# Performance work log

Hardware: AMD Instinct MI355X
Metric: run time of the kernel (lower is better)

Reference implementation:

```python
import jax, jax.numpy as jnp
import numpy as np

K = 3      # kernel size (hardcoded 3x3 in the torch module via repeat(...,9,...))
PAD = 1
STRIDE = 1


def _unfold(x):
    # torch.nn.functional.unfold equivalent: (B,C,H,W) -> (B,C,K,K,oh,ow)
    B, C, H, W = x.shape
    p = jax.lax.conv_general_dilated_patches(
        x, (K, K), (STRIDE, STRIDE), ((PAD, PAD), (PAD, PAD)))
    oh, ow = p.shape[2], p.shape[3]
    return p.reshape(B, C, K, K, oh, ow)


def setup_inputs() -> dict:
    key = jax.random.key(0)
    k1, k2, k3, k4 = jax.random.split(key, 4)
    B, Cin, Cout, H, W = 4, 64, 64, 128, 128
    inputs = jax.random.normal(k1, (B, Cin, H, W), jnp.float32)
    depth = jax.random.uniform(k2, (B, 1, H, W), jnp.float32)  # positive depths
    weight = jax.random.uniform(k3, (K, Cout, Cin, K, K), jnp.float32, minval=-0.05, maxval=0.05)
    bias = jax.random.uniform(k4, (Cout,), jnp.float32, minval=-0.05, maxval=0.05)
    return {"inputs": inputs, "depth": depth, "weight": weight, "bias": bias, "f": 1}


def reference(inputs, depth, weight, bias, f):
    # --- DepthKernelFn: per-depth-plane binary masks ---
    depth_wins = _unfold(depth)          # (B,1,K,K,oh,ow)
    s_wins = depth_wins / f              # grid spacing s_i = d / f
    cy, cx = K // 2, K // 2
    d0 = depth_wins[:, :, cy, cx]        # center depth      (B,1,oh,ow)
    s0 = s_wins[:, :, cy, cx]            # center spacing    (B,1,oh,ow)
    offs = jnp.arange(K, dtype=inputs.dtype) - (K - 1) / 2.0  # l - (K-1)/2
    # z_l at center: d0 + (l-1)*s0  -> (K,B,1,oh,ow)
    z0 = d0[None] + offs[:, None, None, None, None] * s0[None]
    half = s0[None] / 2
    a = (z0 - half)[:, :, :, None, None]  # (K,B,1,1,1,oh,ow)
    b = (z0 + half)[:, :, :, None, None]
    dw = depth_wins[None]                 # (1,B,1,K,K,oh,ow)
    # mask_l = 1 where a <= depth < b else 0  (same as the where-cascade in torch)
    mask = ((dw >= a) & (dw < b)).astype(inputs.dtype)  # (K,B,1,K,K,oh,ow)

    # --- RepeatKernelConvFn: masked windowed conv via einsum ---
    inp_wins = _unfold(inputs)            # (B,C,K,K,oh,ow)
    x = inp_wins[None] * mask             # (K,B,C,K,K,oh,ow), depth C=1 broadcasts
    out = jnp.einsum('hijklmn,hojkl->iomn', x, weight)
    out = out + bias.reshape(1, -1, 1, 1)
    return out
```

## Files before the change

### kernel.cpp

```cpp
#include <hip/hip_runtime.h>
#include <math.h>

#define B_N  4
#define CIN  64
#define COUT 64
#define H_N  128
#define W_N  128

typedef _Float16 half8 __attribute__((ext_vector_type(8)));
typedef float    f32x4 __attribute__((ext_vector_type(4)));

#define KTOT   1728
#define NSTEP  54
#define WA_BYTES ((size_t)NSTEP * 4 * 64 * 8 * 2)

__global__ void wprep(const float* __restrict__ w, _Float16* __restrict__ wa) {
    int idx = blockIdx.x * 256 + threadIdx.x;
    if (idx >= NSTEP * 4 * 64) return;
    int lane = idx & 63;
    int mt   = (idx >> 6) & 3;
    int s    = idx >> 8;
    int m    = mt * 16 + (lane & 15);
    int kl0  = (lane >> 4) * 8;
    _Float16 v[8];
#pragma unroll
    for (int j = 0; j < 8; ++j) {
        int k = s * 32 + kl0 + j;
        int g = k >> 6;
        int c = k & 63;
        int t = g / 3;
        int h = g % 3;
        v[j] = (_Float16)w[(((size_t)(h * COUT) + m) * CIN + c) * 9 + t];
    }
    *(int4*)&wa[(size_t)idx * 8] = *(int4*)v;
}

#define XS_LINE 64
#define XS_ROW  (66 * XS_LINE)

__global__ __launch_bounds__(256, 4)
void conv_mfma(const float* __restrict__ inp, const float* __restrict__ depth,
               const _Float16* __restrict__ wa, const float* __restrict__ bias,
               const int* __restrict__ fptr, float* __restrict__ out) {
    __shared__ _Float16 Xs[3 * XS_ROW];
    __shared__ unsigned hLds[64];

    int bid  = blockIdx.x;
    int xh   = bid & 1;
    int y    = (bid >> 1) & (H_N - 1);
    int b    = bid >> 8;
    int x0   = xh * 64;
    int tid  = threadIdx.x;
    int lane = tid & 63;
    int mq   = tid >> 6;
    int ln15 = lane & 15;
    int quad = lane >> 4;

    {
        int xl  = tid & 63;
        int cq  = tid >> 6;
        int xi  = xl + 1;
        int key = xi & 7;
#pragma unroll
        for (int dyi = 0; dyi < 3; ++dyi) {
            int yy = y + dyi - 1;
            _Float16 hb[16];
            if (yy >= 0 && yy < H_N) {
                const float* src = inp + (((size_t)b * CIN + cq * 16) * H_N + yy) * W_N + (x0 + xl);
                float tf[16];
#pragma unroll
                for (int cc = 0; cc < 16; ++cc) tf[cc] = src[(size_t)cc * H_N * W_N];
#pragma unroll
                for (int cc = 0; cc < 16; ++cc) hb[cc] = (_Float16)tf[cc];
            } else {
#pragma unroll
                for (int cc = 0; cc < 16; ++cc) hb[cc] = (_Float16)0.f;
            }
            _Float16* dst = &Xs[dyi * XS_ROW + xi * XS_LINE];
            *(int4*)&dst[((cq * 2    ) ^ key) * 8] = *(int4*)&hb[0];
            *(int4*)&dst[((cq * 2 + 1) ^ key) * 8] = *(int4*)&hb[8];
        }
        if (tid < 48) {
            int dyi  = tid >> 4;
            int rem  = tid & 15;
            int side = rem >> 3;
            int ck   = rem & 7;
            int xi2  = side ? 65 : 0;
            int xg   = x0 + xi2 - 1;
            int key2 = xi2 & 7;
            int yy   = y + dyi - 1;
            _Float16 hb[8];
            if (xg >= 0 && xg < W_N && yy >= 0 && yy < H_N) {
                const float* src = inp + (((size_t)b * CIN + ck * 8) * H_N + yy) * W_N + xg;
#pragma unroll
                for (int cc = 0; cc < 8; ++cc) hb[cc] = (_Float16)src[(size_t)cc * H_N * W_N];
            } else {
#pragma unroll
                for (int cc = 0; cc < 8; ++cc) hb[cc] = (_Float16)0.f;
            }
            *(int4*)&Xs[dyi * XS_ROW + xi2 * XS_LINE + (ck ^ key2) * 8] = *(int4*)&hb[0];
        }
    }

    const half8* wa8 = (const half8*)wa;
    half8 Abuf[2][6];
    {
        const half8* bA = wa8 + (size_t)mq * 64 + lane;
#pragma unroll
        for (int j = 0; j < 6; ++j) Abuf[0][j] = bA[(size_t)j * 4 * 64];
    }

    if (tid < 64) {
        int x = x0 + tid;
        double fd  = (double)(*fptr);
        float  d0f = depth[((size_t)b * H_N + y) * W_N + x];
        double dd  = (double)d0f;
        double inv = fd / dd;
        bool   pos = (inv > 0.0);
        unsigned pk = 0;
        for (int t = 0; t < 9; ++t) {
            int dy = t / 3 - 1, dx = t % 3 - 1;
            int yy = y + dy, xx = x + dx;
            float dwf = (yy >= 0 && yy < H_N && xx >= 0 && xx < W_N)
                        ? depth[((size_t)b * H_N + yy) * W_N + xx] : 0.f;
            int h = -1;
            if (pos) {
                double u  = ((double)dwf - dd) * inv + 1.5;
                double uf = floor(u);
                if (uf >= 0.0 && uf <= 2.0) h = (int)uf;
            }
            pk |= (unsigned)(h + 1) << (2 * t);
        }
        hLds[tid] = pk;
    }

    __syncthreads();

    unsigned hpk[4];
#pragma unroll
    for (int nt = 0; nt < 4; ++nt) hpk[nt] = hLds[nt * 16 + ln15];

    f32x4 acc[4];
#pragma unroll
    for (int nt = 0; nt < 4; ++nt) acc[nt] = (f32x4){0.f, 0.f, 0.f, 0.f};

    half8 z8 = {(_Float16)0.f, (_Float16)0.f, (_Float16)0.f, (_Float16)0.f,
                (_Float16)0.f, (_Float16)0.f, (_Float16)0.f, (_Float16)0.f};

#pragma unroll
    for (int t = 0; t < 9; ++t) {
        int dyi = t / 3;
        int dx  = t % 3 - 1;

        half8 bb[8];
#pragma unroll
        for (int nt = 0; nt < 4; ++nt) {
            int xs = nt * 16 + ln15 + dx + 1;
            int k2 = xs & 7;
            int ba = dyi * XS_ROW + xs * XS_LINE;
            bb[nt * 2 + 0] = *(const half8*)&Xs[ba + ((quad    ) ^ k2) * 8];
            bb[nt * 2 + 1] = *(const half8*)&Xs[ba + ((quad + 4) ^ k2) * 8];
        }

        if (t < 8) {
            const half8* bA = wa8 + ((size_t)(t + 1) * 24 + mq) * 64 + lane;
#pragma unroll
            for (int j = 0; j < 6; ++j) Abuf[(t + 1) & 1][j] = bA[(size_t)j * 4 * 64];
        }

        int hb[4];
#pragma unroll
        for (int nt = 0; nt < 4; ++nt) hb[nt] = (hpk[nt] >> (2 * t)) & 3;

#pragma unroll
        for (int h = 0; h < 3; ++h) {
#pragma unroll
            for (int kk = 0; kk < 2; ++kk) {
                int j = h * 2 + kk;
#pragma unroll
                for (int nt = 0; nt < 4; ++nt) {
                    half8 c = (hb[nt] == h + 1) ? bb[nt * 2 + kk] : z8;
                    acc[nt] = __builtin_amdgcn_mfma_f32_16x16x32_f16(Abuf[t & 1][j], c, acc[nt], 0, 0, 0);
                }
            }
        }
    }

#pragma unroll
    for (int nt = 0; nt < 4; ++nt) {
        int x = x0 + nt * 16 + ln15;
#pragma unroll
        for (int r = 0; r < 4; ++r) {
            int o = mq * 16 + quad * 4 + r;
            out[(((size_t)b * COUT + o) * H_N + y) * W_N + x] = acc[nt][r] + bias[o];
        }
    }
}

__global__ __launch_bounds__(256)
void conv25d(const float* __restrict__ inp, const float* __restrict__ depth,
             const float* __restrict__ wsrc, const float* __restrict__ bias,
             const int* __restrict__ fptr, float* __restrict__ out) {
    int bid = blockIdx.x;
    int xt  = bid & 3;
    int y   = (bid >> 2) & (H_N - 1);
    int b   = bid >> 9;
    int o   = threadIdx.x & 63;
    int q   = threadIdx.x >> 6;
    int x0  = xt * 32 + q * 8;
    double fd = (double)(*fptr);
    float acc[8];
    float bv = bias[o];
#pragma unroll
    for (int i = 0; i < 8; ++i) acc[i] = bv;
    const float* dcen = depth + ((size_t)b * H_N + y) * W_N;
    float d0[8];
#pragma unroll
    for (int i = 0; i < 8; ++i) d0[i] = dcen[x0 + i];
    for (int t = 0; t < 9; ++t) {
        int dy = t / 3 - 1, dx = t % 3 - 1;
        int yy = y + dy;
        if (yy < 0 || yy >= H_N) continue;
        const float* drow = depth + ((size_t)b * H_N + yy) * W_N;
        int hsel[8];
#pragma unroll
        for (int i = 0; i < 8; ++i) {
            int xx = x0 + i + dx;
            int h = -1;
            if (xx >= 0 && xx < W_N) {
                double dd = (double)d0[i];
                double s0 = dd / fd;
                if (s0 > 0.0) {
                    double u = ((double)drow[xx] - dd) / s0 + 1.5;
                    double uf = floor(u);
                    if (uf >= 0.0 && uf <= 2.0) h = (int)uf;
                }
            }
            hsel[i] = h;
        }
        const float* irow = inp + ((size_t)b * CIN * H_N + yy) * W_N;
        for (int c = 0; c < CIN; ++c) {
            const float* wb = wsrc + ((size_t)o * CIN + c) * 9 + t;
            float w0 = wb[0], w1 = wb[(size_t)COUT * CIN * 9], w2 = wb[2 * (size_t)COUT * CIN * 9];
            const float* ir = irow + (size_t)c * H_N * W_N;
#pragma unroll
            for (int i = 0; i < 8; ++i) {
                int h = hsel[i];
                if (h >= 0) {
                    float wv = (h == 0) ? w0 : ((h == 1) ? w1 : w2);
                    acc[i] = fmaf(ir[x0 + i + dx], wv, acc[i]);
                }
            }
        }
    }
    float* orow = out + (((size_t)b * COUT + o) * H_N + y) * W_N;
#pragma unroll
    for (int i = 0; i < 8; ++i) orow[x0 + i] = acc[i];
}

extern "C" void kernel_launch(void* const* d_in, const int* in_sizes, int n_in,
                              void* d_out, int out_size, void* d_ws, size_t ws_size,
                              hipStream_t stream) {
    const float* inp   = (const float*)d_in[0];
    const float* depth = (const float*)d_in[1];
    const float* w     = (const float*)d_in[2];
    const float* bias  = (const float*)d_in[3];
    const int*   f     = (const int*)d_in[4];
    float* out = (float*)d_out;

    if (ws_size >= WA_BYTES) {
        _Float16* wa = (_Float16*)d_ws;
        wprep<<<NSTEP, 256, 0, stream>>>(w, wa);
        conv_mfma<<<B_N * H_N * 2, 256, 0, stream>>>(inp, depth, wa, bias, f, out);
    } else {
        conv25d<<<B_N * H_N * (W_N / 32), 256, 0, stream>>>(inp, depth, w, bias, f, out);
    }
}
```

Measured before the change: 100.2 us.

## Pipeline input row loads with MFMA compute across kernel rows

```diff
diff --git a/kernel.cpp b/kernel.cpp
--- a/kernel.cpp
+++ b/kernel.cpp
@@ -38,7 +38,7 @@
 #define XS_LINE 64
 #define XS_ROW  (66 * XS_LINE)
 
-__global__ __launch_bounds__(256, 4)
+__global__ __launch_bounds__(256, 3)
 void conv_mfma(const float* __restrict__ inp, const float* __restrict__ depth,
                const _Float16* __restrict__ wa, const float* __restrict__ bias,
                const int* __restrict__ fptr, float* __restrict__ out) {
@@ -56,54 +56,62 @@
     int ln15 = lane & 15;
     int quad = lane >> 4;
 
-    {
-        int xl  = tid & 63;
-        int cq  = tid >> 6;
-        int xi  = xl + 1;
-        int key = xi & 7;
-#pragma unroll
-        for (int dyi = 0; dyi < 3; ++dyi) {
-            int yy = y + dyi - 1;
-            _Float16 hb[16];
-            if (yy >= 0 && yy < H_N) {
-                const float* src = inp + (((size_t)b * CIN + cq * 16) * H_N + yy) * W_N + (x0 + xl);
-                float tf[16];
-#pragma unroll
-                for (int cc = 0; cc < 16; ++cc) tf[cc] = src[(size_t)cc * H_N * W_N];
-#pragma unroll
-                for (int cc = 0; cc < 16; ++cc) hb[cc] = (_Float16)tf[cc];
-            } else {
-#pragma unroll
-                for (int cc = 0; cc < 16; ++cc) hb[cc] = (_Float16)0.f;
-            }
-            _Float16* dst = &Xs[dyi * XS_ROW + xi * XS_LINE];
-            *(int4*)&dst[((cq * 2    ) ^ key) * 8] = *(int4*)&hb[0];
-            *(int4*)&dst[((cq * 2 + 1) ^ key) * 8] = *(int4*)&hb[8];
-        }
-        if (tid < 48) {
-            int dyi  = tid >> 4;
-            int rem  = tid & 15;
-            int side = rem >> 3;
-            int ck   = rem & 7;
-            int xi2  = side ? 65 : 0;
-            int xg   = x0 + xi2 - 1;
-            int key2 = xi2 & 7;
-            int yy   = y + dyi - 1;
-            _Float16 hb[8];
-            if (xg >= 0 && xg < W_N && yy >= 0 && yy < H_N) {
-                const float* src = inp + (((size_t)b * CIN + ck * 8) * H_N + yy) * W_N + xg;
-#pragma unroll
-                for (int cc = 0; cc < 8; ++cc) hb[cc] = (_Float16)src[(size_t)cc * H_N * W_N];
-            } else {
-#pragma unroll
-                for (int cc = 0; cc < 8; ++cc) hb[cc] = (_Float16)0.f;
-            }
-            *(int4*)&Xs[dyi * XS_ROW + xi2 * XS_LINE + (ck ^ key2) * 8] = *(int4*)&hb[0];
-        }
+    int xl   = tid & 63;
+    int cq   = tid >> 6;
+    int xi   = xl + 1;
+    int key  = xi & 7;
+    int side = (tid >> 3) & 1;
+    int ck   = tid & 7;
+    int xi2  = side ? 65 : 0;
+    int xg   = x0 + xi2 - 1;
+    int key2 = xi2 & 7;
+
+    const size_t HW = (size_t)H_N * W_N;
+
+#define LOAD_ROW(dyi, buf, hbuf) {                                            \
+        int yy_ = y + (dyi) - 1;                                              \
+        if (yy_ >= 0 && yy_ < H_N) {                                          \
+            const float* src_ = inp + (((size_t)b * CIN + cq * 16) * H_N + yy_) * W_N + (x0 + xl); \
+            _Pragma("unroll")                                                 \
+            for (int cc = 0; cc < 16; ++cc) buf[cc] = src_[(size_t)cc * HW];  \
+        } else {                                                              \
+            _Pragma("unroll")                                                 \
+            for (int cc = 0; cc < 16; ++cc) buf[cc] = 0.f;                    \
+        }                                                                     \
+        if (tid < 16) {                                                       \
+            if (xg >= 0 && xg < W_N && yy_ >= 0 && yy_ < H_N) {               \
+                const float* hsrc_ = inp + (((size_t)b * CIN + ck * 8) * H_N + yy_) * W_N + xg; \
+                _Pragma("unroll")                                             \
+                for (int cc = 0; cc < 8; ++cc) hbuf[cc] = hsrc_[(size_t)cc * HW]; \
+            } else {                                                          \
+                _Pragma("unroll")                                             \
+                for (int cc = 0; cc < 8; ++cc) hbuf[cc] = 0.f;                \
+            }                                                                 \
+        }                                                                     \
+    }
+
+#define WRITE_ROW(dyi, buf, hbuf) {                                           \
+        _Float16 hb_[16];                                                     \
+        _Pragma("unroll")                                                     \
+        for (int cc = 0; cc < 16; ++cc) hb_[cc] = (_Float16)buf[cc];          \
+        _Float16* dst_ = &Xs[(dyi) * XS_ROW + xi * XS_LINE];                  \
+        *(int4*)&dst_[((cq * 2    ) ^ key) * 8] = *(int4*)&hb_[0];            \
+        *(int4*)&dst_[((cq * 2 + 1) ^ key) * 8] = *(int4*)&hb_[8];            \
+        if (tid < 16) {                                                       \
+            _Float16 hh_[8];                                                  \
+            _Pragma("unroll")                                                 \
+            for (int cc = 0; cc < 8; ++cc) hh_[cc] = (_Float16)hbuf[cc];      \
+            *(int4*)&Xs[(dyi) * XS_ROW + xi2 * XS_LINE + (ck ^ key2) * 8] = *(int4*)&hh_[0]; \
+        }                                                                     \
     }
 
     const half8* wa8 = (const half8*)wa;
     half8 Abuf[2][6];
+
+    float rbuf[16];
+    float rhbuf[8];
+    LOAD_ROW(0, rbuf, rhbuf);
+
     {
         const half8* bA = wa8 + (size_t)mq * 64 + lane;
 #pragma unroll
@@ -134,6 +142,7 @@
         hLds[tid] = pk;
     }
 
+    WRITE_ROW(0, rbuf, rhbuf);
     __syncthreads();
 
     unsigned hpk[4];
@@ -148,51 +157,65 @@
                 (_Float16)0.f, (_Float16)0.f, (_Float16)0.f, (_Float16)0.f};
 
 #pragma unroll
-    for (int t = 0; t < 9; ++t) {
-        int dyi = t / 3;
-        int dx  = t % 3 - 1;
-
-        half8 bb[8];
-#pragma unroll
-        for (int nt = 0; nt < 4; ++nt) {
-            int xs = nt * 16 + ln15 + dx + 1;
-            int k2 = xs & 7;
-            int ba = dyi * XS_ROW + xs * XS_LINE;
-            bb[nt * 2 + 0] = *(const half8*)&Xs[ba + ((quad    ) ^ k2) * 8];
-            bb[nt * 2 + 1] = *(const half8*)&Xs[ba + ((quad + 4) ^ k2) * 8];
-        }
-
-        if (t < 8) {
-            const half8* bA = wa8 + ((size_t)(t + 1) * 24 + mq) * 64 + lane;
-#pragma unroll
-            for (int j = 0; j < 6; ++j) Abuf[(t + 1) & 1][j] = bA[(size_t)j * 4 * 64];
-        }
-
-        int hb[4];
-#pragma unroll
-        for (int nt = 0; nt < 4; ++nt) hb[nt] = (hpk[nt] >> (2 * t)) & 3;
-
-#pragma unroll
-        for (int h = 0; h < 3; ++h) {
-#pragma unroll
-            for (int kk = 0; kk < 2; ++kk) {
-                int j = h * 2 + kk;
-#pragma unroll
-                for (int nt = 0; nt < 4; ++nt) {
-                    half8 c = (hb[nt] == h + 1) ? bb[nt * 2 + kk] : z8;
-                    acc[nt] = __builtin_amdgcn_mfma_f32_16x16x32_f16(Abuf[t & 1][j], c, acc[nt], 0, 0, 0);
+    for (int r = 0; r < 3; ++r) {
+        float nbuf[16];
+        float nhbuf[8];
+        if (r < 2) LOAD_ROW(r + 1, nbuf, nhbuf);
+
+#pragma unroll
+        for (int dxl = 0; dxl < 3; ++dxl) {
+            int t  = r * 3 + dxl;
+            int dx = dxl - 1;
+
+            half8 bb[8];
+#pragma unroll
+            for (int nt = 0; nt < 4; ++nt) {
+                int xs = nt * 16 + ln15 + dx + 1;
+                int k2 = xs & 7;
+                int ba = r * XS_ROW + xs * XS_LINE;
+                bb[nt * 2 + 0] = *(const half8*)&Xs[ba + ((quad    ) ^ k2) * 8];
+                bb[nt * 2 + 1] = *(const half8*)&Xs[ba + ((quad + 4) ^ k2) * 8];
+            }
+
+            if (t < 8) {
+                const half8* bA = wa8 + ((size_t)(t + 1) * 24 + mq) * 64 + lane;
+#pragma unroll
+                for (int j = 0; j < 6; ++j) Abuf[(t + 1) & 1][j] = bA[(size_t)j * 4 * 64];
+            }
+
+            int hb[4];
+#pragma unroll
+            for (int nt = 0; nt < 4; ++nt) hb[nt] = (hpk[nt] >> (2 * t)) & 3;
+
+#pragma unroll
+            for (int h = 0; h < 3; ++h) {
+#pragma unroll
+                for (int kk = 0; kk < 2; ++kk) {
+                    int j = h * 2 + kk;
+#pragma unroll
+                    for (int nt = 0; nt < 4; ++nt) {
+                        half8 c = (hb[nt] == h + 1) ? bb[nt * 2 + kk] : z8;
+                        acc[nt] = __builtin_amdgcn_mfma_f32_16x16x32_f16(Abuf[t & 1][j], c, acc[nt], 0, 0, 0);
+                    }
                 }
             }
         }
-    }
+
+        if (r < 2) {
+            WRITE_ROW(r + 1, nbuf, nhbuf);
+            __syncthreads();
+        }
+    }
+#undef LOAD_ROW
+#undef WRITE_ROW
 
 #pragma unroll
     for (int nt = 0; nt < 4; ++nt) {
         int x = x0 + nt * 16 + ln15;
 #pragma unroll
-        for (int r = 0; r < 4; ++r) {
-            int o = mq * 16 + quad * 4 + r;
-            out[(((size_t)b * COUT + o) * H_N + y) * W_N + x] = acc[nt][r] + bias[o];
+        for (int rr = 0; rr < 4; ++rr) {
+            int o = mq * 16 + quad * 4 + rr;
+            out[(((size_t)b * COUT + o) * H_N + y) * W_N + x] = acc[nt][rr] + bias[o];
         }
     }
 }
```

New measurement: 99.50 us. About the same (-0.6%).
